# Kernel tuning notes

Measured on AMD Instinct MI355X. Metric: run time of the kernel, lower is better.

## Reference

```python
import jax, jax.numpy as jnp
import numpy as np

N = 100_000   # nodes
E = 1_600_000 # edges (avg degree 16)
B = 512       # graphs in batch
F_IN = 64; H = 4; D = 64; HD = H * D; EXTRA = 16
NEG_SLOPE = 0.2  # DGL GATConv default


def _gat_conv(x, src, dst, W, al, ar, bias):
    """DGL GATConv: fc -> per-head attn logits -> edge leaky_relu -> segment softmax over dst -> scatter-sum."""
    h = (x @ W).reshape(N, H, D)                       # [N,H,D]
    el = jnp.sum(h * al, axis=-1)                      # [N,H]
    er = jnp.sum(h * ar, axis=-1)                      # [N,H]
    e = jax.nn.leaky_relu(el[src] + er[dst], NEG_SLOPE)  # [E,H]
    m = jax.ops.segment_max(e, dst, num_segments=N)    # [N,H]
    m = jnp.where(jnp.isfinite(m), m, 0.0)             # guard empty segments
    ex = jnp.exp(e - m[dst])                           # [E,H]
    den = jax.ops.segment_sum(ex, dst, num_segments=N) # [N,H]
    alpha = ex / jnp.maximum(den[dst], 1e-9)           # [E,H]
    msg = h[src] * alpha[:, :, None]                   # [E,H,D]
    out = jax.ops.segment_sum(msg, dst, num_segments=N) + bias.reshape(1, H, D)
    return out  # [N,H,D]


def setup_inputs() -> dict:
    key = jax.random.key(0)
    ks = jax.random.split(key, 26)
    nrm = lambda k, shape: jax.random.normal(k, shape, dtype=jnp.float32) * 0.5
    src = jax.random.randint(ks[0], (E,), 0, N)
    # ensure every node has >=1 incoming edge (DGL disallows zero in-degree by default)
    dst = jnp.concatenate([jnp.arange(N), jax.random.randint(ks[1], (E - N,), 0, N)])
    node_graph = jnp.sort(jax.random.randint(ks[2], (N,), 0, B))
    inp = dict(
        src=src, dst=dst, node_graph=node_graph,
        feats_node=jax.random.normal(ks[3], (N, F_IN), dtype=jnp.float32),
        feats_graph=jax.random.normal(ks[4], (B, EXTRA), dtype=jnp.float32),
        W1=nrm(ks[5], (F_IN, HD)), al1=nrm(ks[6], (H, D)), ar1=nrm(ks[7], (H, D)), bg1=jnp.zeros(HD),
        W2=nrm(ks[8], (HD, HD)),  al2=nrm(ks[9], (H, D)), ar2=nrm(ks[10], (H, D)), bg2=jnp.zeros(HD),
        W3=nrm(ks[11], (HD, HD)), al3=nrm(ks[12], (H, D)), ar3=nrm(ks[13], (H, D)), bg3=jnp.zeros(HD),
        sw=nrm(ks[14], (HD, 1)), sb=jnp.zeros(1),
        lw1=nrm(ks[15], (HD + EXTRA, 2 * D)), lb1=jnp.zeros(2 * D),
        lw2=nrm(ks[16], (2 * D, D)), lb2=jnp.zeros(D),
        lw3=nrm(ks[17], (D, 1)), lb3=jnp.zeros(1),
    )
    return inp


def reference(src, dst, node_graph, feats_node, feats_graph,
              W1, al1, ar1, bg1, W2, al2, ar2, bg2, W3, al3, ar3, bg3,
              sw, sb, lw1, lb1, lw2, lb2, lw3, lb3):
    selu = jax.nn.selu
    x = selu(_gat_conv(feats_node, src, dst, W1, al1, ar1, bg1)).reshape(N, HD)
    x = selu(_gat_conv(x, src, dst, W2, al2, ar2, bg2)).reshape(N, HD)
    x = selu(_gat_conv(x, src, dst, W3, al3, ar3, bg3)).reshape(N, HD)
    # WeightedAverage readout: sigmoid-scored weighted mean per graph
    w = jax.nn.sigmoid(x @ sw + sb)                               # [N,1]
    num = jax.ops.segment_sum(w * x, node_graph, num_segments=B)  # [B,HD]
    den = jax.ops.segment_sum(w, node_graph, num_segments=B)      # [B,1]
    emb = num / jnp.maximum(den, 1e-9)
    y = jnp.concatenate([emb, feats_graph], axis=1)
    y = selu(y @ lw1 + lb1)
    y = selu(y @ lw2 + lb2)
    return y @ lw3 + lb3  # [B,1]
```

## Files before the change

kernel.cpp:

```cpp
#include <hip/hip_runtime.h>

#define N_NODES 100000
#define N_EDGES 1600000
#define N_GRAPHS 512
#define F_IN 64
#define HD 256
#define EXTRA 16
#define SCAN_BLOCK 512

typedef float f32x4 __attribute__((ext_vector_type(4)));
typedef _Float16 f16x4 __attribute__((ext_vector_type(4)));
typedef _Float16 f16x8 __attribute__((ext_vector_type(8)));

__device__ __forceinline__ float selu_f(float x) {
    const float a = 1.6732632423543772f, sc = 1.0507009873554805f;
    return x > 0.f ? sc * x : sc * a * (__expf(x) - 1.f);
}

__global__ __launch_bounds__(256) void hist_k(const int* __restrict__ dst, int* __restrict__ hist) {
    int j = blockIdx.x * 256 + threadIdx.x;
    if (j < N_EDGES) atomicAdd(&hist[dst[j]], 1);
}

__global__ __launch_bounds__(SCAN_BLOCK) void scan1_k(const int* __restrict__ hist,
                                                      int* __restrict__ row_ptr,
                                                      int* __restrict__ bsums) {
    __shared__ int sm[SCAN_BLOCK];
    int t = threadIdx.x;
    int i = blockIdx.x * SCAN_BLOCK + t;
    int v = (i < N_NODES) ? hist[i] : 0;
    sm[t] = v;
    __syncthreads();
    for (int off = 1; off < SCAN_BLOCK; off <<= 1) {
        int add = (t >= off) ? sm[t - off] : 0;
        __syncthreads();
        sm[t] += add;
        __syncthreads();
    }
    if (i < N_NODES) row_ptr[i] = sm[t] - v;
    if (t == SCAN_BLOCK - 1) bsums[blockIdx.x] = sm[t];
}

__global__ __launch_bounds__(256) void scan23_k(int* __restrict__ row_ptr, const int* __restrict__ bsums,
                                                int* __restrict__ cursor, int nb) {
    __shared__ int bs[256];
    int t = threadIdx.x;
    bs[t] = (t < nb) ? bsums[t] : 0;
    __syncthreads();
    for (int off = 1; off < 256; off <<= 1) {
        int add = (t >= off) ? bs[t - off] : 0;
        __syncthreads();
        bs[t] += add;
        __syncthreads();
    }
    int i = blockIdx.x * 256 + t;
    if (i < N_NODES) {
        int b = i / SCAN_BLOCK;
        int p = b > 0 ? bs[b - 1] : 0;
        int r = row_ptr[i] + p;
        row_ptr[i] = r;
        cursor[i] = r;
    }
    if (i == 0) row_ptr[N_NODES] = N_EDGES;
}

__global__ __launch_bounds__(256) void scatter_k(const int* __restrict__ src,
                                                 const int* __restrict__ dst,
                                                 int* __restrict__ cursor,
                                                 int* __restrict__ csr_src) {
    int j = blockIdx.x * 256 + threadIdx.x;
    if (j < N_EDGES) {
        int r = atomicAdd(&cursor[dst[j]], 1);
        csr_src[r] = src[j];
    }
}

__device__ __forceinline__ void wsplit(const float* __restrict__ W, _Float16* __restrict__ Wh,
                                       _Float16* __restrict__ Wl, int idx, int K) {
    int n = idx / K, k = idx - n * K;
    float w = W[(size_t)k * HD + n];
    _Float16 hi = (_Float16)w;
    Wh[idx] = hi;
    Wl[idx] = (_Float16)(w - (float)hi);
}

__global__ __launch_bounds__(256) void prep_k(const float* __restrict__ W1,
                                              const float* __restrict__ W2,
                                              const float* __restrict__ W3,
                                              _Float16* __restrict__ W1h, _Float16* __restrict__ W1l,
                                              _Float16* __restrict__ W2h, _Float16* __restrict__ W2l,
                                              _Float16* __restrict__ W3h, _Float16* __restrict__ W3l,
                                              const int* __restrict__ node_graph,
                                              int* __restrict__ gstart) {
    int b = blockIdx.x, t = threadIdx.x;
    if (b < 64) {
        wsplit(W1, W1h, W1l, b * 256 + t, F_IN);
    } else if (b < 320) {
        wsplit(W2, W2h, W2l, (b - 64) * 256 + t, HD);
    } else if (b < 576) {
        wsplit(W3, W3h, W3l, (b - 320) * 256 + t, HD);
    } else {
        int g = (b - 576) * 256 + t;
        if (g > N_GRAPHS) return;
        int lo = 0, hi = N_NODES;
        while (lo < hi) {
            int mid = (lo + hi) >> 1;
            if (node_graph[mid] < g) lo = mid + 1; else hi = mid;
        }
        gstart[g] = lo;
    }
}

template <int K, bool F32A>
__global__ __launch_bounds__(256) void gemm_split_k(const void* __restrict__ Aptr,
                                                    const _Float16* __restrict__ Alo_p,
                                                    const _Float16* __restrict__ Bt_hi,
                                                    const _Float16* __restrict__ Bt_lo,
                                                    const float* __restrict__ al,
                                                    const float* __restrict__ ar,
                                                    _Float16* __restrict__ Chi,
                                                    float* __restrict__ el,
                                                    float* __restrict__ er, int M) {
    const int BM = 64, BN = 128, LDP = 40;
    __shared__ union {
        struct {
            _Float16 Ash[BM][LDP];
            _Float16 Asl[BM][LDP];
            _Float16 Bsh[BN][LDP];
            _Float16 Bsl[BN][LDP];
        } s;
        _Float16 ctile[BM][BN];
    } u;
    __shared__ float pl[4][64];
    __shared__ float pr[4][64];
    _Float16 (&Ash)[BM][LDP] = u.s.Ash;
    _Float16 (&Asl)[BM][LDP] = u.s.Asl;
    _Float16 (&Bsh)[BN][LDP] = u.s.Bsh;
    _Float16 (&Bsl)[BN][LDP] = u.s.Bsl;

    int tid = threadIdx.x;
    int w = tid >> 6, lane = tid & 63;
    int q = lane >> 4, l16 = lane & 15;
    int row0 = blockIdx.y * BM, col0 = blockIdx.x * BN;
    f32x4 acc[4][2] = {};

    int ar_ = tid >> 2, ao = (tid & 3) * 8;
    f16x8 rAh, rAl, rBh[2], rBl[2];

    auto load_tile = [&](int k0) {
        int gr = row0 + ar_;
        if constexpr (F32A) {
            const float* A32 = (const float*)Aptr;
            float vv[8] = {};
            if (gr < M) {
                float4 va = *(const float4*)(A32 + (size_t)gr * K + k0 + ao);
                float4 vb = *(const float4*)(A32 + (size_t)gr * K + k0 + ao + 4);
                vv[0] = va.x; vv[1] = va.y; vv[2] = va.z; vv[3] = va.w;
                vv[4] = vb.x; vv[5] = vb.y; vv[6] = vb.z; vv[7] = vb.w;
            }
            f16x8 h, l;
#pragma unroll
            for (int i = 0; i < 8; i++) {
                h[i] = (_Float16)vv[i];
                l[i] = (_Float16)(vv[i] - (float)h[i]);
            }
            rAh = h; rAl = l;
        } else {
            const _Float16* Ahi = (const _Float16*)Aptr;
            f16x8 vh = {}, vl = {};
            if (gr < M) {
                vh = *(const f16x8*)(Ahi + (size_t)gr * K + k0 + ao);
                vl = *(const f16x8*)(Alo_p + (size_t)gr * K + k0 + ao);
            }
            rAh = vh; rAl = vl;
        }
#pragma unroll
        for (int c = 0; c < 2; c++) {
            int cc = tid + c * 256;
            int br = cc >> 2, bo = (cc & 3) * 8;
            int gb = col0 + br;
            rBh[c] = *(const f16x8*)(Bt_hi + (size_t)gb * K + k0 + bo);
            rBl[c] = *(const f16x8*)(Bt_lo + (size_t)gb * K + k0 + bo);
        }
    };
    auto store_tile = [&]() {
        *(f16x8*)&Ash[ar_][ao] = rAh;
        *(f16x8*)&Asl[ar_][ao] = rAl;
#pragma unroll
        for (int c = 0; c < 2; c++) {
            int cc = tid + c * 256;
            int br = cc >> 2, bo = (cc & 3) * 8;
            *(f16x8*)&Bsh[br][bo] = rBh[c];
            *(f16x8*)&Bsl[br][bo] = rBl[c];
        }
    };

    load_tile(0);
    store_tile();
    __syncthreads();

    for (int k0 = 0; k0 < K; k0 += 32) {
        bool more = (k0 + 32) < K;
        if (more) load_tile(k0 + 32);

        f16x8 ah[4], alo2[4], bh[2], bl[2];
#pragma unroll
        for (int mf = 0; mf < 4; mf++) {
            int m = mf * 16 + l16;
            ah[mf] = *(const f16x8*)&Ash[m][q * 8];
            alo2[mf] = *(const f16x8*)&Asl[m][q * 8];
        }
#pragma unroll
        for (int nf = 0; nf < 2; nf++) {
            int n = w * 32 + nf * 16 + l16;
            bh[nf] = *(const f16x8*)&Bsh[n][q * 8];
            bl[nf] = *(const f16x8*)&Bsl[n][q * 8];
        }
#pragma unroll
        for (int mf = 0; mf < 4; mf++)
#pragma unroll
            for (int nf = 0; nf < 2; nf++) {
                acc[mf][nf] = __builtin_amdgcn_mfma_f32_16x16x32_f16(ah[mf], bh[nf], acc[mf][nf], 0, 0, 0);
                acc[mf][nf] = __builtin_amdgcn_mfma_f32_16x16x32_f16(ah[mf], bl[nf], acc[mf][nf], 0, 0, 0);
                acc[mf][nf] = __builtin_amdgcn_mfma_f32_16x16x32_f16(alo2[mf], bh[nf], acc[mf][nf], 0, 0, 0);
            }
        if (more) {
            __syncthreads();
            store_tile();
            __syncthreads();
        }
    }

    __syncthreads();

    const int hh = (col0 >> 6) + (w >> 1);
    float alv[2], arv[2];
#pragma unroll
    for (int nf = 0; nf < 2; nf++) {
        int d = (w & 1) * 32 + nf * 16 + l16;
        alv[nf] = al[hh * 64 + d];
        arv[nf] = ar[hh * 64 + d];
    }
#pragma unroll
    for (int mf = 0; mf < 4; mf++) {
#pragma unroll
        for (int i = 0; i < 4; i++) {
            int rl = mf * 16 + q * 4 + i;
            float e_l = 0.f, e_r = 0.f;
#pragma unroll
            for (int nf = 0; nf < 2; nf++) {
                float v = acc[mf][nf][i];
                u.ctile[rl][w * 32 + nf * 16 + l16] = (_Float16)v;
                e_l = fmaf(v, alv[nf], e_l);
                e_r = fmaf(v, arv[nf], e_r);
            }
#pragma unroll
            for (int off = 1; off < 16; off <<= 1) {
                e_l += __shfl_xor(e_l, off, 64);
                e_r += __shfl_xor(e_r, off, 64);
            }
            if (l16 == 0) {
                pl[w][rl] = e_l;
                pr[w][rl] = e_r;
            }
        }
    }
    __syncthreads();
#pragma unroll
    for (int j = 0; j < 4; j++) {
        int c = tid + j * 256;
        int rr2 = c >> 4, co = (c & 15) * 8;
        int gr = row0 + rr2;
        if (gr < M)
            *(f16x8*)(Chi + (size_t)gr * HD + col0 + co) = *(const f16x8*)&u.ctile[rr2][co];
    }
    int h2 = (tid >> 6) & 1, rr = tid & 63;
    int grow = row0 + rr;
    if (grow < M) {
        if (tid < 128) el[(size_t)grow * 4 + (col0 >> 6) + h2] = pl[2 * h2][rr] + pl[2 * h2 + 1][rr];
        else           er[(size_t)grow * 4 + (col0 >> 6) + h2] = pr[2 * h2][rr] + pr[2 * h2 + 1][rr];
    }
}

template <int OUT>
__global__ __launch_bounds__(256) void gat_aggregate_k(const _Float16* __restrict__ hb,
                                                       const float* __restrict__ el,
                                                       const float* __restrict__ er,
                                                       const int* __restrict__ csr_src,
                                                       const int* __restrict__ row_ptr,
                                                       const float* __restrict__ bias,
                                                       _Float16* __restrict__ xhi,
                                                       _Float16* __restrict__ xlo,
                                                       float* __restrict__ xf32,
                                                       const float* __restrict__ sw,
                                                       const float* __restrict__ sb,
                                                       float* __restrict__ wsc) {
    __shared__ float wlds[4][64][4];
    __shared__ int snlds[4][64];
    int wv = threadIdx.x >> 6;
    int lane = threadIdx.x & 63;
    int v = blockIdx.x * 4 + wv;
    bool valid = v < N_NODES;
    int vc = valid ? v : 0;
    int rs = row_ptr[vc];
    int deg = valid ? row_ptr[vc + 1] - rs : 0;
    float4 erv = make_float4(0.f, 0.f, 0.f, 0.f);
    if (valid) erv = *(const float4*)(er + (size_t)vc * 4);

    const int eo = lane >> 5;
    const int fl = lane & 31;
    const int headf = fl >> 3;

    float a[8] = {};
    float dw = 0.f;
    f16x8 hv_pre[4];
    float m_h = 0.f, er_h = 0.f;

    if (deg <= 64) {
        float e0 = -1e30f, e1 = -1e30f, e2 = -1e30f, e3 = -1e30f;
        int my_sn = 0;
        if (lane < deg) {
            my_sn = csr_src[rs + lane];
            float4 elv = *(const float4*)(el + (size_t)my_sn * 4);
            float t0 = elv.x + erv.x, t1 = elv.y + erv.y, t2 = elv.z + erv.z, t3 = elv.w + erv.w;
            e0 = t0 > 0.f ? t0 : 0.2f * t0;
            e1 = t1 > 0.f ? t1 : 0.2f * t1;
            e2 = t2 > 0.f ? t2 : 0.2f * t2;
            e3 = t3 > 0.f ? t3 : 0.2f * t3;
        }
#pragma unroll
        for (int u = 0; u < 4; u++) {
            int pidx = 2 * u + eo;
            int cidx = pidx < deg ? pidx : (deg > 0 ? deg - 1 : 0);
            int snb = __shfl(my_sn, cidx, 64);
            hv_pre[u] = *(const f16x8*)(hb + (size_t)snb * HD + fl * 8);
        }
        float m0 = e0, m1 = e1, m2 = e2, m3 = e3;
        for (int off = 1; off < deg; off <<= 1) {
            m0 = fmaxf(m0, __shfl_xor(m0, off, 64));
            m1 = fmaxf(m1, __shfl_xor(m1, off, 64));
            m2 = fmaxf(m2, __shfl_xor(m2, off, 64));
            m3 = fmaxf(m3, __shfl_xor(m3, off, 64));
        }
        if (lane < deg) {
            wlds[wv][lane][0] = __expf(e0 - m0);
            wlds[wv][lane][1] = __expf(e1 - m1);
            wlds[wv][lane][2] = __expf(e2 - m2);
            wlds[wv][lane][3] = __expf(e3 - m3);
            snlds[wv][lane] = my_sn;
        }

#pragma unroll
        for (int u = 0; u < 4; u++) {
            int idx = 2 * u + eo;
            float w = (idx < deg) ? wlds[wv][idx][headf] : 0.f;
            dw += w;
#pragma unroll
            for (int i = 0; i < 8; i++) a[i] = fmaf(w, (float)hv_pre[u][i], a[i]);
        }
        int t = 8;
        for (; t + 8 <= deg; t += 8) {
            int sn_[4];
            float w_[4];
#pragma unroll
            for (int u = 0; u < 4; u++) {
                int idx = t + 2 * u + eo;
                sn_[u] = snlds[wv][idx];
                w_[u] = wlds[wv][idx][headf];
            }
            f16x8 hv[4];
#pragma unroll
            for (int u = 0; u < 4; u++)
                hv[u] = *(const f16x8*)(hb + (size_t)sn_[u] * HD + fl * 8);
#pragma unroll
            for (int u = 0; u < 4; u++) {
                dw += w_[u];
#pragma unroll
                for (int i = 0; i < 8; i++) a[i] = fmaf(w_[u], (float)hv[u][i], a[i]);
            }
        }
        for (; t < deg; t += 2) {
            int idx = t + eo;
            int cidx = idx < deg ? idx : idx - 1;
            int sn = snlds[wv][cidx];
            float w = (idx < deg) ? wlds[wv][cidx][headf] : 0.f;
            f16x8 hv = *(const f16x8*)(hb + (size_t)sn * HD + fl * 8);
            dw += w;
#pragma unroll
            for (int i = 0; i < 8; i++) a[i] = fmaf(w, (float)hv[i], a[i]);
        }
    } else {
        float m[4] = {-1e30f, -1e30f, -1e30f, -1e30f};
        float s[4] = {0.f, 0.f, 0.f, 0.f};
        for (int t = lane; t < deg; t += 64) {
            int sn = csr_src[rs + t];
            float4 elv = *(const float4*)(el + (size_t)sn * 4);
            float e[4];
            e[0] = elv.x + erv.x; e[1] = elv.y + erv.y; e[2] = elv.z + erv.z; e[3] = elv.w + erv.w;
#pragma unroll
            for (int hh = 0; hh < 4; hh++) {
                float ev = e[hh] > 0.f ? e[hh] : 0.2f * e[hh];
                float mn = fmaxf(m[hh], ev);
                s[hh] = s[hh] * __expf(m[hh] - mn) + __expf(ev - mn);
                m[hh] = mn;
            }
        }
#pragma unroll
        for (int off = 32; off >= 1; off >>= 1) {
#pragma unroll
            for (int hh = 0; hh < 4; hh++) {
                float mo = __shfl_xor(m[hh], off, 64);
                float so = __shfl_xor(s[hh], off, 64);
                float mn = fmaxf(m[hh], mo);
                s[hh] = s[hh] * __expf(m[hh] - mn) + so * __expf(mo - mn);
                m[hh] = mn;
            }
        }
        m_h = headf == 0 ? m[0] : headf == 1 ? m[1] : headf == 2 ? m[2] : m[3];
        float dh = headf == 0 ? s[0] : headf == 1 ? s[1] : headf == 2 ? s[2] : s[3];
        er_h = headf == 0 ? erv.x : headf == 1 ? erv.y : headf == 2 ? erv.z : erv.w;
        dw = (eo == 0) ? dh : 0.f;

        for (int t = 0; t < deg; t += 2) {
            int idx = t + eo;
            int cidx = idx < deg ? idx : idx - 1;
            int sn = csr_src[rs + cidx];
            float w = 0.f;
            if (idx < deg) {
                float e = el[(size_t)sn * 4 + headf] + er_h;
                e = e > 0.f ? e : 0.2f * e;
                w = __expf(e - m_h);
            }
            f16x8 hv = *(const f16x8*)(hb + (size_t)sn * HD + fl * 8);
#pragma unroll
            for (int i = 0; i < 8; i++) a[i] = fmaf(w, (float)hv[i], a[i]);
        }
    }

#pragma unroll
    for (int i = 0; i < 8; i++) a[i] += __shfl_xor(a[i], 32, 64);
    dw += __shfl_xor(dw, 32, 64);
    float inv_den = 1.f / fmaxf(dw, 1e-9f);

    float4 bv0 = *(const float4*)(bias + fl * 8);
    float4 bv1 = *(const float4*)(bias + fl * 8 + 4);
    float o[8];
    o[0] = selu_f(fmaf(a[0], inv_den, bv0.x));
    o[1] = selu_f(fmaf(a[1], inv_den, bv0.y));
    o[2] = selu_f(fmaf(a[2], inv_den, bv0.z));
    o[3] = selu_f(fmaf(a[3], inv_den, bv0.w));
    o[4] = selu_f(fmaf(a[4], inv_den, bv1.x));
    o[5] = selu_f(fmaf(a[5], inv_den, bv1.y));
    o[6] = selu_f(fmaf(a[6], inv_den, bv1.z));
    o[7] = selu_f(fmaf(a[7], inv_den, bv1.w));

    if constexpr (OUT == 0) {
        if (valid) {
            if (eo == 0) {
                f16x8 oh;
#pragma unroll
                for (int i = 0; i < 8; i++) oh[i] = (_Float16)o[i];
                *(f16x8*)(xhi + (size_t)v * HD + fl * 8) = oh;
            } else {
                f16x8 ol;
#pragma unroll
                for (int i = 0; i < 8; i++) {
                    _Float16 hi = (_Float16)o[i];
                    ol[i] = (_Float16)(o[i] - (float)hi);
                }
                *(f16x8*)(xlo + (size_t)v * HD + fl * 8) = ol;
            }
        }
    } else {
        float p;
        if (eo == 0) {
            if (valid) *(float4*)(xf32 + (size_t)v * HD + fl * 8) = make_float4(o[0], o[1], o[2], o[3]);
            float4 sv = *(const float4*)(sw + fl * 8);
            p = o[0] * sv.x + o[1] * sv.y + o[2] * sv.z + o[3] * sv.w;
        } else {
            if (valid) *(float4*)(xf32 + (size_t)v * HD + fl * 8 + 4) = make_float4(o[4], o[5], o[6], o[7]);
            float4 sv = *(const float4*)(sw + fl * 8 + 4);
            p = o[4] * sv.x + o[5] * sv.y + o[6] * sv.z + o[7] * sv.w;
        }
#pragma unroll
        for (int off = 1; off < 64; off <<= 1) p += __shfl_xor(p, off, 64);
        if (lane == 0 && valid) wsc[v] = 1.f / (1.f + __expf(-(p + sb[0])));
    }
}

__global__ __launch_bounds__(256) void readout_part_k(const float* __restrict__ x,
                                                      const float* __restrict__ wsc,
                                                      const int* __restrict__ gstart,
                                                      float* __restrict__ y0p) {
    int g = blockIdx.x >> 2, c = blockIdx.x & 3;
    int f = threadIdx.x;
    int s0 = gstart[g], e0 = gstart[g + 1];
    int len = e0 - s0;
    int cs = s0 + (len * c) / 4, ce = s0 + (len * (c + 1)) / 4;
    float num = 0.f, den = 0.f;
#pragma unroll 4
    for (int n = cs; n < ce; n++) {
        float wn = wsc[n];
        num = fmaf(wn, x[(size_t)n * HD + f], num);
        den += wn;
    }
    float* dst = y0p + (size_t)(g * 4 + c) * 257;
    dst[f] = num;
    if (f == 0) dst[256] = den;
}

__global__ __launch_bounds__(128) void mlp_k(const float* __restrict__ y0p,
                                             const float* __restrict__ fg,
                                             const float* __restrict__ lw1, const float* __restrict__ lb1,
                                             const float* __restrict__ lw2, const float* __restrict__ lb2,
                                             const float* __restrict__ lw3, const float* __restrict__ lb3,
                                             float* __restrict__ out) {
    __shared__ float y0s[272];
    __shared__ float y1s[128];
    int g = blockIdx.x, t = threadIdx.x;
    const float* p0 = y0p + (size_t)(g * 4 + 0) * 257;
    const float* p1 = y0p + (size_t)(g * 4 + 1) * 257;
    const float* p2 = y0p + (size_t)(g * 4 + 2) * 257;
    const float* p3 = y0p + (size_t)(g * 4 + 3) * 257;
    float den = p0[256] + p1[256] + p2[256] + p3[256];
    float invden = 1.f / fmaxf(den, 1e-9f);
    for (int i = t; i < 256; i += 128)
        y0s[i] = (p0[i] + p1[i] + p2[i] + p3[i]) * invden;
    if (t < EXTRA) y0s[256 + t] = fg[g * EXTRA + t];
    __syncthreads();
    float acc = lb1[t];
    for (int k = 0; k < 272; k++) acc = fmaf(y0s[k], lw1[k * 128 + t], acc);
    y1s[t] = selu_f(acc);
    __syncthreads();
    if (t < 64) {
        float a2 = lb2[t];
        for (int k = 0; k < 128; k++) a2 = fmaf(y1s[k], lw2[k * 64 + t], a2);
        float v2 = selu_f(a2);
        float p = v2 * lw3[t];
#pragma unroll
        for (int off = 1; off < 64; off <<= 1) p += __shfl_xor(p, off, 64);
        if (t == 0) out[g] = p + lb3[0];
    }
}

extern "C" void kernel_launch(void* const* d_in, const int* in_sizes, int n_in,
                              void* d_out, int out_size, void* d_ws, size_t ws_size,
                              hipStream_t stream) {
    const int* src = (const int*)d_in[0];
    const int* dst = (const int*)d_in[1];
    const int* node_graph = (const int*)d_in[2];
    const float* feats_node = (const float*)d_in[3];
    const float* feats_graph = (const float*)d_in[4];
    const float* W1 = (const float*)d_in[5];
    const float* al1 = (const float*)d_in[6];
    const float* ar1 = (const float*)d_in[7];
    const float* bg1 = (const float*)d_in[8];
    const float* W2 = (const float*)d_in[9];
    const float* al2 = (const float*)d_in[10];
    const float* ar2 = (const float*)d_in[11];
    const float* bg2 = (const float*)d_in[12];
    const float* W3 = (const float*)d_in[13];
    const float* al3 = (const float*)d_in[14];
    const float* ar3 = (const float*)d_in[15];
    const float* bg3 = (const float*)d_in[16];
    const float* sw = (const float*)d_in[17];
    const float* sb = (const float*)d_in[18];
    const float* lw1 = (const float*)d_in[19];
    const float* lb1 = (const float*)d_in[20];
    const float* lw2 = (const float*)d_in[21];
    const float* lb2 = (const float*)d_in[22];
    const float* lw3 = (const float*)d_in[23];
    const float* lb3 = (const float*)d_in[24];
    float* out = (float*)d_out;

    char* ws = (char*)d_ws;
    size_t off = 0;
    auto alloc = [&](size_t bytes) -> char* {
        char* p = ws + off;
        off += (bytes + 255) & ~(size_t)255;
        return p;
    };
    _Float16* xhi = (_Float16*)alloc((size_t)N_NODES * HD * 2);
    _Float16* xlo = (_Float16*)alloc((size_t)N_NODES * HD * 2);
    float* xf32 = (float*)xhi;
    _Float16* hhi = (_Float16*)alloc((size_t)N_NODES * HD * 2);
    _Float16* W1hi = (_Float16*)alloc((size_t)F_IN * HD * 2);
    _Float16* W1lo = (_Float16*)alloc((size_t)F_IN * HD * 2);
    _Float16* W2hi = (_Float16*)alloc((size_t)HD * HD * 2);
    _Float16* W2lo = (_Float16*)alloc((size_t)HD * HD * 2);
    _Float16* W3hi = (_Float16*)alloc((size_t)HD * HD * 2);
    _Float16* W3lo = (_Float16*)alloc((size_t)HD * HD * 2);
    float* el = (float*)alloc((size_t)N_NODES * 4 * 4);
    float* er = (float*)alloc((size_t)N_NODES * 4 * 4);
    float* wsc = (float*)alloc((size_t)N_NODES * 4);
    float* y0p = (float*)alloc((size_t)N_GRAPHS * 4 * 257 * 4);
    int* hist = (int*)alloc((size_t)N_NODES * 4);
    int* row_ptr = (int*)alloc((size_t)(N_NODES + 1) * 4);
    int* cursor = (int*)alloc((size_t)N_NODES * 4);
    int* csr_src = (int*)alloc((size_t)N_EDGES * 4);
    int* gstart = (int*)alloc((size_t)(N_GRAPHS + 1) * 4);
    int* bsums = (int*)alloc(256 * 4);
    (void)ws_size; (void)in_sizes; (void)n_in; (void)out_size;

    hipMemsetAsync(hist, 0, (size_t)N_NODES * 4, stream);

    hist_k<<<(N_EDGES + 255) / 256, 256, 0, stream>>>(dst, hist);
    int nb = (N_NODES + SCAN_BLOCK - 1) / SCAN_BLOCK;
    scan1_k<<<nb, SCAN_BLOCK, 0, stream>>>(hist, row_ptr, bsums);
    scan23_k<<<(N_NODES + 255) / 256, 256, 0, stream>>>(row_ptr, bsums, cursor, nb);
    scatter_k<<<(N_EDGES + 255) / 256, 256, 0, stream>>>(src, dst, cursor, csr_src);

    prep_k<<<579, 256, 0, stream>>>(W1, W2, W3, W1hi, W1lo, W2hi, W2lo, W3hi, W3lo, node_graph, gstart);

    dim3 ggrid(HD / 128, (N_NODES + 63) / 64);
    int nwb = (N_NODES + 3) / 4;

    gemm_split_k<F_IN, true><<<ggrid, 256, 0, stream>>>((const void*)feats_node, nullptr, W1hi, W1lo, al1, ar1, hhi, el, er, N_NODES);
    gat_aggregate_k<0><<<nwb, 256, 0, stream>>>(hhi, el, er, csr_src, row_ptr, bg1, xhi, xlo, nullptr, nullptr, nullptr, nullptr);
    gemm_split_k<HD, false><<<ggrid, 256, 0, stream>>>((const void*)xhi, xlo, W2hi, W2lo, al2, ar2, hhi, el, er, N_NODES);
    gat_aggregate_k<0><<<nwb, 256, 0, stream>>>(hhi, el, er, csr_src, row_ptr, bg2, xhi, xlo, nullptr, nullptr, nullptr, nullptr);
    gemm_split_k<HD, false><<<ggrid, 256, 0, stream>>>((const void*)xhi, xlo, W3hi, W3lo, al3, ar3, hhi, el, er, N_NODES);
    gat_aggregate_k<1><<<nwb, 256, 0, stream>>>(hhi, el, er, csr_src, row_ptr, bg3, nullptr, nullptr, xf32, sw, sb, wsc);

    readout_part_k<<<N_GRAPHS * 4, 256, 0, stream>>>(xf32, wsc, gstart, y0p);
    mlp_k<<<N_GRAPHS, 128, 0, stream>>>(y0p, feats_graph, lw1, lb1, lw2, lb2, lw3, lb3, out);
}
```

Baseline: 915.8 us.

## Drop low-half activation split in layer 2/3 GEMMs and pipeline neighbor gathers

```diff
diff --git a/kernel.cpp b/kernel.cpp
--- a/kernel.cpp
+++ b/kernel.cpp
@@ -111,7 +111,7 @@
     }
 }
 
-template <int K, bool F32A>
+template <int K, bool F32A, int ATERMS>
 __global__ __launch_bounds__(256) void gemm_split_k(const void* __restrict__ Aptr,
                                                     const _Float16* __restrict__ Alo_p,
                                                     const _Float16* __restrict__ Bt_hi,
@@ -167,12 +167,14 @@
             rAh = h; rAl = l;
         } else {
             const _Float16* Ahi = (const _Float16*)Aptr;
-            f16x8 vh = {}, vl = {};
+            f16x8 vh = {};
             if (gr < M) {
                 vh = *(const f16x8*)(Ahi + (size_t)gr * K + k0 + ao);
-                vl = *(const f16x8*)(Alo_p + (size_t)gr * K + k0 + ao);
-            }
-            rAh = vh; rAl = vl;
+                if constexpr (ATERMS == 3) rAl = *(const f16x8*)(Alo_p + (size_t)gr * K + k0 + ao);
+            } else if constexpr (ATERMS == 3) {
+                rAl = f16x8{};
+            }
+            rAh = vh;
         }
 #pragma unroll
         for (int c = 0; c < 2; c++) {
@@ -185,7 +187,7 @@
     };
     auto store_tile = [&]() {
         *(f16x8*)&Ash[ar_][ao] = rAh;
-        *(f16x8*)&Asl[ar_][ao] = rAl;
+        if constexpr (ATERMS == 3) *(f16x8*)&Asl[ar_][ao] = rAl;
 #pragma unroll
         for (int c = 0; c < 2; c++) {
             int cc = tid + c * 256;
@@ -208,7 +210,7 @@
         for (int mf = 0; mf < 4; mf++) {
             int m = mf * 16 + l16;
             ah[mf] = *(const f16x8*)&Ash[m][q * 8];
-            alo2[mf] = *(const f16x8*)&Asl[m][q * 8];
+            if constexpr (ATERMS == 3) alo2[mf] = *(const f16x8*)&Asl[m][q * 8];
         }
 #pragma unroll
         for (int nf = 0; nf < 2; nf++) {
@@ -222,7 +224,8 @@
             for (int nf = 0; nf < 2; nf++) {
                 acc[mf][nf] = __builtin_amdgcn_mfma_f32_16x16x32_f16(ah[mf], bh[nf], acc[mf][nf], 0, 0, 0);
                 acc[mf][nf] = __builtin_amdgcn_mfma_f32_16x16x32_f16(ah[mf], bl[nf], acc[mf][nf], 0, 0, 0);
-                acc[mf][nf] = __builtin_amdgcn_mfma_f32_16x16x32_f16(alo2[mf], bh[nf], acc[mf][nf], 0, 0, 0);
+                if constexpr (ATERMS == 3)
+                    acc[mf][nf] = __builtin_amdgcn_mfma_f32_16x16x32_f16(alo2[mf], bh[nf], acc[mf][nf], 0, 0, 0);
             }
         if (more) {
             __syncthreads();
@@ -290,7 +293,6 @@
                                                        const int* __restrict__ row_ptr,
                                                        const float* __restrict__ bias,
                                                        _Float16* __restrict__ xhi,
-                                                       _Float16* __restrict__ xlo,
                                                        float* __restrict__ xf32,
                                                        const float* __restrict__ sw,
                                                        const float* __restrict__ sb,
@@ -313,7 +315,6 @@
 
     float a[8] = {};
     float dw = 0.f;
-    f16x8 hv_pre[4];
     float m_h = 0.f, er_h = 0.f;
 
     if (deg <= 64) {
@@ -328,12 +329,17 @@
             e2 = t2 > 0.f ? t2 : 0.2f * t2;
             e3 = t3 > 0.f ? t3 : 0.2f * t3;
         }
+        int P = (deg + 1) >> 1;
+        f16x8 hv[8];
+        int pA = P < 4 ? P : 4;
 #pragma unroll
         for (int u = 0; u < 4; u++) {
-            int pidx = 2 * u + eo;
-            int cidx = pidx < deg ? pidx : (deg > 0 ? deg - 1 : 0);
-            int snb = __shfl(my_sn, cidx, 64);
-            hv_pre[u] = *(const f16x8*)(hb + (size_t)snb * HD + fl * 8);
+            if (u < pA) {
+                int idx = 2 * u + eo;
+                int cidx = idx < deg ? idx : deg - 1;
+                int snb = __shfl(my_sn, cidx, 64);
+                hv[u] = *(const f16x8*)(hb + (size_t)snb * HD + fl * 8);
+            }
         }
         float m0 = e0, m1 = e1, m2 = e2, m3 = e3;
         for (int off = 1; off < deg; off <<= 1) {
@@ -350,44 +356,33 @@
             snlds[wv][lane] = my_sn;
         }
 
-#pragma unroll
-        for (int u = 0; u < 4; u++) {
-            int idx = 2 * u + eo;
-            float w = (idx < deg) ? wlds[wv][idx][headf] : 0.f;
-            dw += w;
-#pragma unroll
-            for (int i = 0; i < 8; i++) a[i] = fmaf(w, (float)hv_pre[u][i], a[i]);
-        }
-        int t = 8;
-        for (; t + 8 <= deg; t += 8) {
-            int sn_[4];
-            float w_[4];
-#pragma unroll
-            for (int u = 0; u < 4; u++) {
-                int idx = t + 2 * u + eo;
-                sn_[u] = snlds[wv][idx];
-                w_[u] = wlds[wv][idx][headf];
-            }
-            f16x8 hv[4];
-#pragma unroll
-            for (int u = 0; u < 4; u++)
-                hv[u] = *(const f16x8*)(hb + (size_t)sn_[u] * HD + fl * 8);
-#pragma unroll
-            for (int u = 0; u < 4; u++) {
-                dw += w_[u];
-#pragma unroll
-                for (int i = 0; i < 8; i++) a[i] = fmaf(w_[u], (float)hv[u][i], a[i]);
-            }
-        }
-        for (; t < deg; t += 2) {
-            int idx = t + eo;
-            int cidx = idx < deg ? idx : idx - 1;
-            int sn = snlds[wv][cidx];
-            float w = (idx < deg) ? wlds[wv][cidx][headf] : 0.f;
-            f16x8 hv = *(const f16x8*)(hb + (size_t)sn * HD + fl * 8);
-            dw += w;
-#pragma unroll
-            for (int i = 0; i < 8; i++) a[i] = fmaf(w, (float)hv[i], a[i]);
+        int pB = P < 8 ? P : 8;
+#pragma unroll
+        for (int u = 4; u < 8; u++) {
+            if (u < pB) {
+                int idx = 2 * u + eo;
+                int cidx = idx < deg ? idx : deg - 1;
+                hv[u] = *(const f16x8*)(hb + (size_t)snlds[wv][cidx] * HD + fl * 8);
+            }
+        }
+        for (int pb = 0; pb < P; pb += 8) {
+#pragma unroll
+            for (int j = 0; j < 8; j++) {
+                int p = pb + j;
+                if (p >= P) break;
+                int idx = 2 * p + eo;
+                float w = (idx < deg) ? wlds[wv][idx][headf] : 0.f;
+                dw += w;
+                f16x8 h = hv[j];
+#pragma unroll
+                for (int i = 0; i < 8; i++) a[i] = fmaf(w, (float)h[i], a[i]);
+                int pn = p + 8;
+                if (pn < P) {
+                    int idx2 = 2 * pn + eo;
+                    int cidx2 = idx2 < deg ? idx2 : deg - 1;
+                    hv[j] = *(const f16x8*)(hb + (size_t)snlds[wv][cidx2] * HD + fl * 8);
+                }
+            }
         }
     } else {
         float m[4] = {-1e30f, -1e30f, -1e30f, -1e30f};
@@ -455,21 +450,11 @@
     o[7] = selu_f(fmaf(a[7], inv_den, bv1.w));
 
     if constexpr (OUT == 0) {
-        if (valid) {
-            if (eo == 0) {
-                f16x8 oh;
-#pragma unroll
-                for (int i = 0; i < 8; i++) oh[i] = (_Float16)o[i];
-                *(f16x8*)(xhi + (size_t)v * HD + fl * 8) = oh;
-            } else {
-                f16x8 ol;
-#pragma unroll
-                for (int i = 0; i < 8; i++) {
-                    _Float16 hi = (_Float16)o[i];
-                    ol[i] = (_Float16)(o[i] - (float)hi);
-                }
-                *(f16x8*)(xlo + (size_t)v * HD + fl * 8) = ol;
-            }
+        if (valid && eo == 0) {
+            f16x8 oh;
+#pragma unroll
+            for (int i = 0; i < 8; i++) oh[i] = (_Float16)o[i];
+            *(f16x8*)(xhi + (size_t)v * HD + fl * 8) = oh;
         }
     } else {
         float p;
@@ -581,8 +566,9 @@
         return p;
     };
     _Float16* xhi = (_Float16*)alloc((size_t)N_NODES * HD * 2);
-    _Float16* xlo = (_Float16*)alloc((size_t)N_NODES * HD * 2);
+    char* xpad = alloc((size_t)N_NODES * HD * 2);
     float* xf32 = (float*)xhi;
+    (void)xpad;
     _Float16* hhi = (_Float16*)alloc((size_t)N_NODES * HD * 2);
     _Float16* W1hi = (_Float16*)alloc((size_t)F_IN * HD * 2);
     _Float16* W1lo = (_Float16*)alloc((size_t)F_IN * HD * 2);
@@ -615,12 +601,12 @@
     dim3 ggrid(HD / 128, (N_NODES + 63) / 64);
     int nwb = (N_NODES + 3) / 4;
 
-    gemm_split_k<F_IN, true><<<ggrid, 256, 0, stream>>>((const void*)feats_node, nullptr, W1hi, W1lo, al1, ar1, hhi, el, er, N_NODES);
-    gat_aggregate_k<0><<<nwb, 256, 0, stream>>>(hhi, el, er, csr_src, row_ptr, bg1, xhi, xlo, nullptr, nullptr, nullptr, nullptr);
-    gemm_split_k<HD, false><<<ggrid, 256, 0, stream>>>((const void*)xhi, xlo, W2hi, W2lo, al2, ar2, hhi, el, er, N_NODES);
-    gat_aggregate_k<0><<<nwb, 256, 0, stream>>>(hhi, el, er, csr_src, row_ptr, bg2, xhi, xlo, nullptr, nullptr, nullptr, nullptr);
-    gemm_split_k<HD, false><<<ggrid, 256, 0, stream>>>((const void*)xhi, xlo, W3hi, W3lo, al3, ar3, hhi, el, er, N_NODES);
-    gat_aggregate_k<1><<<nwb, 256, 0, stream>>>(hhi, el, er, csr_src, row_ptr, bg3, nullptr, nullptr, xf32, sw, sb, wsc);
+    gemm_split_k<F_IN, true, 3><<<ggrid, 256, 0, stream>>>((const void*)feats_node, nullptr, W1hi, W1lo, al1, ar1, hhi, el, er, N_NODES);
+    gat_aggregate_k<0><<<nwb, 256, 0, stream>>>(hhi, el, er, csr_src, row_ptr, bg1, xhi, nullptr, nullptr, nullptr, nullptr);
+    gemm_split_k<HD, false, 2><<<ggrid, 256, 0, stream>>>((const void*)xhi, nullptr, W2hi, W2lo, al2, ar2, hhi, el, er, N_NODES);
+    gat_aggregate_k<0><<<nwb, 256, 0, stream>>>(hhi, el, er, csr_src, row_ptr, bg2, xhi, nullptr, nullptr, nullptr, nullptr);
+    gemm_split_k<HD, false, 2><<<ggrid, 256, 0, stream>>>((const void*)xhi, nullptr, W3hi, W3lo, al3, ar3, hhi, el, er, N_NODES);
+    gat_aggregate_k<1><<<nwb, 256, 0, stream>>>(hhi, el, er, csr_src, row_ptr, bg3, nullptr, xf32, sw, sb, wsc);
 
     readout_part_k<<<N_GRAPHS * 4, 256, 0, stream>>>(xf32, wsc, gstart, y0p);
     mlp_k<<<N_GRAPHS, 128, 0, stream>>>(y0p, feats_graph, lw1, lb1, lw2, lb2, lw3, lb3, out);
```

New measurement: 886.0 us. -3.3%, faster.
